# Kernel tuning notes

Measured on AMD Instinct MI355X. Metric: run time of the kernel, lower is better.

Reference implementation:

```python
import jax, jax.numpy as jnp
import numpy as np

W, B, S, D = 4, 1, 1024, 1024   # simulated world_size, batch, local seq, embed_dim
H, DS, HM = 16, 64, 4            # num_heads, summary_dim, meta_heads


def mha(q, k, v, w_in, b_in, w_out, b_out, nheads):
    """torch nn.MultiheadAttention (batch_first). Returns (out, head-averaged weights)."""
    d = q.shape[-1]
    hd = d // nheads
    wq, wk, wv = jnp.split(w_in, 3, axis=0)
    bq, bk, bv = jnp.split(b_in, 3)
    Bq, Sq, _ = q.shape
    Sk = k.shape[1]
    qh = (q @ wq.T + bq).reshape(Bq, Sq, nheads, hd)
    kh = (k @ wk.T + bk).reshape(Bq, Sk, nheads, hd)
    vh = (v @ wv.T + bv).reshape(Bq, Sk, nheads, hd)
    scores = jnp.einsum('bqhd,bkhd->bhqk', qh, kh) / float(np.sqrt(hd))
    attn = jax.nn.softmax(scores, axis=-1)
    out = jnp.einsum('bhqk,bkhd->bqhd', attn, vh).reshape(Bq, Sq, d)
    return out @ w_out.T + b_out, attn.mean(axis=1)


def attn_stats(attn):
    """attn: (B, S) -> (B, 4) [entropy, gini, max, top5]."""
    ent = -(attn * jnp.log(attn + 1e-8)).sum(-1, keepdims=True)
    s = jnp.sort(attn, axis=-1)
    n = attn.shape[-1]
    idx = jnp.arange(1, n + 1, dtype=attn.dtype)
    gini = 2.0 * (idx * s).sum(-1) / (n * s.sum(-1) + 1e-8) - (n + 1) / n
    mx = attn.max(-1, keepdims=True)
    k = min(5, n)
    top5 = jax.lax.top_k(attn, k)[0].sum(-1, keepdims=True)
    return jnp.concatenate([ent, gini[..., None], mx, top5], axis=-1)


def _forward(x, local_in_w, local_in_b, local_out_w, local_out_b,
             sum_query, sum_in_w, sum_in_b, sum_out_w, sum_out_b,
             pat_w1, pat_b1, pat_w2, pat_b2, comb_w, comb_b,
             meta_in_w, meta_in_b, meta_out_w, meta_out_b,
             route_w1, route_b1, route_w2, route_b2,
             cross_in_w, cross_in_b, cross_out_w, cross_out_b,
             gate_w, gate_b, proj_w, proj_b):
    nW = x.shape[0]

    # 1) local attention per rank: (W,B,S,D)
    local = jax.vmap(lambda xc: mha(xc, xc, xc, local_in_w, local_in_b,
                                    local_out_w, local_out_b, H)[0])(x)

    # 2) chunk summary per rank
    def summarize(lo):
        q = jnp.broadcast_to(sum_query, (lo.shape[0], 1, lo.shape[-1]))
        content, w = mha(q, lo, lo, sum_in_w, sum_in_b, sum_out_w, sum_out_b, H)
        content, w = content[:, 0], w[:, 0]              # (B,D), (B,S)
        pat = attn_stats(w)                               # (B,4)
        pat = jax.nn.relu(pat @ pat_w1.T + pat_b1) @ pat_w2.T + pat_b2
        return jnp.concatenate([content, pat], axis=-1) @ comb_w.T + comb_b

    summaries = jax.vmap(summarize)(local)                # (W,B,DS)
    all_sum = jnp.transpose(summaries, (1, 0, 2))         # (B,W,DS) = all-gather

    # 3) meta attention over chunk summaries -> routing weights
    refined, chunk_attn = mha(all_sum, all_sum, all_sum,
                              meta_in_w, meta_in_b, meta_out_w, meta_out_b, HM)
    logits = (jax.nn.relu(refined @ route_w1.T + route_b1) @ route_w2.T + route_b2)[..., 0]
    routing = jax.nn.softmax(logits, axis=-1)             # (B,W)

    all_chunks = jnp.transpose(local, (1, 0, 2, 3))       # (B,W,S,D) = all-gather

    # 4) selective cross-attention + gated combine, per rank
    def per_rank(r, lo):
        rm = routing * (1.0 - jax.nn.one_hot(r, nW, dtype=routing.dtype))
        rm = rm / (rm.sum(-1, keepdims=True) + 1e-8)
        kv = jnp.einsum('bw,bwsd->bsd', rm, all_chunks)
        cross, _ = mha(lo, kv, kv, cross_in_w, cross_in_b, cross_out_w, cross_out_b, H)
        g = jax.nn.sigmoid(jnp.concatenate([lo, cross], axis=-1) @ gate_w.T + gate_b)
        comb = g * cross + (1.0 - g) * lo
        return comb @ proj_w.T + proj_b

    out = jax.vmap(per_rank)(jnp.arange(nW), local)       # (W,B,S,D)
    return out


def setup_inputs() -> dict:
    key = jax.random.key(0)
    ks = iter(jax.random.split(key, 40))
    p = lambda *shape: jax.random.normal(next(ks), shape, dtype=jnp.float32) * 0.02
    inp = {
        'x': jax.random.normal(next(ks), (W, B, S, D), dtype=jnp.float32),
        'local_in_w': p(3 * D, D), 'local_in_b': p(3 * D),
        'local_out_w': p(D, D), 'local_out_b': p(D),
        'sum_query': p(1, 1, D),
        'sum_in_w': p(3 * D, D), 'sum_in_b': p(3 * D),
        'sum_out_w': p(D, D), 'sum_out_b': p(D),
        'pat_w1': p(DS, 4), 'pat_b1': p(DS),
        'pat_w2': p(DS, DS), 'pat_b2': p(DS),
        'comb_w': p(DS, D + DS), 'comb_b': p(DS),
        'meta_in_w': p(3 * DS, DS), 'meta_in_b': p(3 * DS),
        'meta_out_w': p(DS, DS), 'meta_out_b': p(DS),
        'route_w1': p(DS, DS), 'route_b1': p(DS),
        'route_w2': p(1, DS), 'route_b2': p(1),
        'cross_in_w': p(3 * D, D), 'cross_in_b': p(3 * D),
        'cross_out_w': p(D, D), 'cross_out_b': p(D),
        'gate_w': p(D, 2 * D), 'gate_b': p(D),
        'proj_w': p(D, D), 'proj_b': p(D),
    }
    return inp


def reference(x, local_in_w, local_in_b, local_out_w, local_out_b,
              sum_query, sum_in_w, sum_in_b, sum_out_w, sum_out_b,
              pat_w1, pat_b1, pat_w2, pat_b2, comb_w, comb_b,
              meta_in_w, meta_in_b, meta_out_w, meta_out_b,
              route_w1, route_b1, route_w2, route_b2,
              cross_in_w, cross_in_b, cross_out_w, cross_out_b,
              gate_w, gate_b, proj_w, proj_b):
    return _forward(x, local_in_w, local_in_b, local_out_w, local_out_b,
                    sum_query, sum_in_w, sum_in_b, sum_out_w, sum_out_b,
                    pat_w1, pat_b1, pat_w2, pat_b2, comb_w, comb_b,
                    meta_in_w, meta_in_b, meta_out_w, meta_out_b,
                    route_w1, route_b1, route_w2, route_b2,
                    cross_in_w, cross_in_b, cross_out_w, cross_out_b,
                    gate_w, gate_b, proj_w, proj_b)
```

## Files before the change

### kernel.cpp

```cpp
#include <hip/hip_runtime.h>
#include <hip/hip_bf16.h>
#include <stdint.h>

typedef uint16_t u16;
typedef __attribute__((ext_vector_type(8))) short short8;
typedef __attribute__((ext_vector_type(8))) unsigned short ushort8;
typedef __attribute__((ext_vector_type(4))) float f32x4;

#define AS1 __attribute__((address_space(1)))
#define AS3 __attribute__((address_space(3)))

__device__ __forceinline__ float b2f(u16 u){
  union{uint32_t i; float f;} v; v.i=((uint32_t)u)<<16; return v.f;
}
__device__ __forceinline__ u16 f2b(float f){
  union{uint32_t i; float f;} v; v.f=f;
  return (u16)((v.i + 0x7fffu + ((v.i>>16)&1u))>>16);
}
__device__ __forceinline__ u16 f2bf(float f){
  __hip_bfloat16 h = __float2bfloat16(f);
  return *reinterpret_cast<u16*>(&h);
}

struct CvtP { const float* src[8]; u16* dst[8]; long n[8]; };
__global__ void cvt_multi(CvtP p) {
  const int seg = blockIdx.y;
  const long i = ((long)blockIdx.x*256 + threadIdx.x)*8;
  if (i >= p.n[seg]) return;
  const float* in = p.src[seg];
  float4 a = *(const float4*)&in[i];
  float4 b = *(const float4*)&in[i+4];
  ushort8 o;
  o[0]=f2b(a.x); o[1]=f2b(a.y); o[2]=f2b(a.z); o[3]=f2b(a.w);
  o[4]=f2b(b.x); o[5]=f2b(b.y); o[6]=f2b(b.z); o[7]=f2b(b.w);
  *(ushort8*)&p.dst[seg][i] = o;
}

struct GemmP {
  const u16* A; const u16* B; u16* C; const float* bias;
  const u16* B2; u16* C2; const float* bias2;
  long lda, ldb, ldc, ldb2, ldc2;
  int K, Nstore, Nstore2, ySplit, act, outf;
  float scale;
};

__global__ __launch_bounds__(512) void gemm_nt(GemmP p) {
  __shared__ __align__(16) u16 lA[2][4096];
  __shared__ __align__(16) u16 lB[2][4096];
  const int t = threadIdx.x;
  const int wave = t >> 6, lane = t & 63;
  int by = blockIdx.y;
  const u16* Bp; u16* Cp; const float* bias; long ldb, ldc; int nst;
  if (by >= p.ySplit) {
    by -= p.ySplit; Bp = p.B2; Cp = p.C2; bias = p.bias2;
    ldb = p.ldb2; ldc = p.ldc2; nst = p.Nstore2;
  } else {
    Bp = p.B; Cp = p.C; bias = p.bias; ldb = p.ldb; ldc = p.ldc; nst = p.Nstore;
  }
  const u16* A = p.A + (long)blockIdx.x * 128 * p.lda;
  const u16* B = Bp + (long)by * 128 * ldb;
  const int srow = t >> 2, skk = (t & 3) * 8;
  const int wr = wave >> 2, wc = wave & 3;
  const int fr = lane & 15, fk = (lane >> 4) * 8;
  f32x4 acc[4][2] = {};

  __builtin_amdgcn_global_load_lds((const AS1 void*)(A + (long)srow*p.lda + skk),
                                   (AS3 void*)&lA[0][t*8], 16, 0, 0);
  __builtin_amdgcn_global_load_lds((const AS1 void*)(B + (long)srow*ldb + skk),
                                   (AS3 void*)&lB[0][t*8], 16, 0, 0);
  __syncthreads();
  int cur = 0;
  for (int k0 = 0; k0 < p.K; k0 += 32) {
    if (k0 + 32 < p.K) {
      const int nb = cur ^ 1, kn = k0 + 32;
      __builtin_amdgcn_global_load_lds((const AS1 void*)(A + (long)srow*p.lda + kn + skk),
                                       (AS3 void*)&lA[nb][t*8], 16, 0, 0);
      __builtin_amdgcn_global_load_lds((const AS1 void*)(B + (long)srow*ldb + kn + skk),
                                       (AS3 void*)&lB[nb][t*8], 16, 0, 0);
    }
    short8 av[4], bv[2];
    #pragma unroll
    for (int mi = 0; mi < 4; ++mi) av[mi] = *(const short8*)&lA[cur][(wr*64 + mi*16 + fr)*32 + fk];
    #pragma unroll
    for (int ni = 0; ni < 2; ++ni) bv[ni] = *(const short8*)&lB[cur][(wc*32 + ni*16 + fr)*32 + fk];
    #pragma unroll
    for (int mi = 0; mi < 4; ++mi)
      #pragma unroll
      for (int ni = 0; ni < 2; ++ni)
        acc[mi][ni] = __builtin_amdgcn_mfma_f32_16x16x32_bf16(av[mi], bv[ni], acc[mi][ni], 0, 0, 0);
    __syncthreads();
    cur ^= 1;
  }

  const int rbase = blockIdx.x*128 + wr*64;
  const int cbase = by*128 + wc*32;
  const int rsub = (lane >> 4) * 4;
  #pragma unroll
  for (int ni = 0; ni < 2; ++ni) {
    const int col = cbase + ni*16 + fr;
    if (col >= nst) continue;
    const float bs = bias ? bias[col] : 0.f;
    #pragma unroll
    for (int mi = 0; mi < 4; ++mi) {
      #pragma unroll
      for (int j = 0; j < 4; ++j) {
        float v = acc[mi][ni][j] * p.scale + bs;
        if (p.act == 1) v = 1.f / (1.f + __expf(-v));
        const long idx = (long)(rbase + mi*16 + rsub + j) * ldc + col;
        if (p.outf) ((float*)Cp)[idx] = v;
        else        Cp[idx] = f2b(v);
      }
    }
  }
}

struct FlashP {
  const u16 *q, *k, *v; u16* o;
  long ldq, ldkv, ldo;
  long qB, kvB, oB;
};

__global__ __launch_bounds__(256) void flash_k(FlashP p) {
  const int t = threadIdx.x, w4 = t >> 6, lane = t & 63;
  const int qt = blockIdx.x, h = blockIdx.y, wz = blockIdx.z;
  const int fr = lane & 15, g = lane >> 4, fk = g * 8;
  __shared__ __align__(16) u16 kt[64][72];
  __shared__ __align__(16) u16 vt[64][72];
  __shared__ __align__(16) u16 pl[4][16][72];

  const u16* Q = p.q + (long)wz*p.qB + (long)(qt*64 + w4*16)*p.ldq + h*64;
  const u16* K = p.k + (long)wz*p.kvB + h*64;
  const u16* V = p.v + (long)wz*p.kvB + h*64;

  short8 aq[2];
  aq[0] = *(const short8*)&Q[(long)fr*p.ldq + fk];
  aq[1] = *(const short8*)&Q[(long)fr*p.ldq + 32 + fk];

  f32x4 acc[4] = {};
  float mst[4], lst[4];
  #pragma unroll
  for (int j = 0; j < 4; ++j) { mst[j] = -3e38f; lst[j] = 0.f; }

  const int krow = t >> 2, kseg = (t & 3) * 16;
  const int vp = t & 31, vc = (t >> 5) * 8;

  short8 kr0, kr1, vr0, vr1;
  kr0 = *(const short8*)&K[(long)krow*p.ldkv + kseg];
  kr1 = *(const short8*)&K[(long)krow*p.ldkv + kseg + 8];
  vr0 = *(const short8*)&V[(long)(2*vp)*p.ldkv + vc];
  vr1 = *(const short8*)&V[(long)(2*vp + 1)*p.ldkv + vc];

  for (int it = 0; it < 16; ++it) {
    *(short8*)&kt[krow][kseg]     = kr0;
    *(short8*)&kt[krow][kseg + 8] = kr1;
    #pragma unroll
    for (int e = 0; e < 8; ++e) {
      const uint32_t pk = (uint32_t)(uint16_t)vr0[e] | ((uint32_t)(uint16_t)vr1[e] << 16);
      *(uint32_t*)&vt[vc + e][2*vp] = pk;
    }
    __syncthreads();

    if (it + 1 < 16) {
      const int kn = (it + 1) * 64;
      kr0 = *(const short8*)&K[(long)(kn + krow)*p.ldkv + kseg];
      kr1 = *(const short8*)&K[(long)(kn + krow)*p.ldkv + kseg + 8];
      vr0 = *(const short8*)&V[(long)(kn + 2*vp)*p.ldkv + vc];
      vr1 = *(const short8*)&V[(long)(kn + 2*vp + 1)*p.ldkv + vc];
    }

    f32x4 s[4] = {};
    __builtin_amdgcn_s_setprio(1);
    #pragma unroll
    for (int ni = 0; ni < 4; ++ni) {
      short8 bk0 = *(const short8*)&kt[ni*16 + fr][fk];
      short8 bk1 = *(const short8*)&kt[ni*16 + fr][32 + fk];
      s[ni] = __builtin_amdgcn_mfma_f32_16x16x32_bf16(aq[0], bk0, s[ni], 0, 0, 0);
      s[ni] = __builtin_amdgcn_mfma_f32_16x16x32_bf16(aq[1], bk1, s[ni], 0, 0, 0);
    }
    __builtin_amdgcn_s_setprio(0);
    #pragma unroll
    for (int ni = 0; ni < 4; ++ni) s[ni] *= 0.125f;

    #pragma unroll
    for (int j = 0; j < 4; ++j) {
      float rm = fmaxf(fmaxf(s[0][j], s[1][j]), fmaxf(s[2][j], s[3][j]));
      #pragma unroll
      for (int o = 8; o; o >>= 1) rm = fmaxf(rm, __shfl_xor(rm, o, 64));
      const float mnew = fmaxf(mst[j], rm);
      const float alpha = __expf(mst[j] - mnew);
      float rs = 0.f;
      #pragma unroll
      for (int ni = 0; ni < 4; ++ni) {
        const float pv = __expf(s[ni][j] - mnew);
        s[ni][j] = pv;
        rs += pv;
      }
      #pragma unroll
      for (int o = 8; o; o >>= 1) rs += __shfl_xor(rs, o, 64);
      lst[j] = lst[j]*alpha + rs;
      mst[j] = mnew;
      #pragma unroll
      for (int nv = 0; nv < 4; ++nv) acc[nv][j] *= alpha;
    }

    #pragma unroll
    for (int ni = 0; ni < 4; ++ni)
      #pragma unroll
      for (int j = 0; j < 4; ++j)
        pl[w4][g*4 + j][ni*16 + fr] = f2bf(s[ni][j]);

    __builtin_amdgcn_s_setprio(1);
    #pragma unroll
    for (int ks = 0; ks < 2; ++ks) {
      short8 pa = *(const short8*)&pl[w4][fr][ks*32 + fk];
      #pragma unroll
      for (int nv = 0; nv < 4; ++nv) {
        short8 bvv = *(const short8*)&vt[nv*16 + fr][ks*32 + fk];
        acc[nv] = __builtin_amdgcn_mfma_f32_16x16x32_bf16(pa, bvv, acc[nv], 0, 0, 0);
      }
    }
    __builtin_amdgcn_s_setprio(0);
    __syncthreads();
  }

  u16* O = p.o + (long)wz*p.oB + (long)(qt*64 + w4*16)*p.ldo + h*64;
  #pragma unroll
  for (int j = 0; j < 4; ++j) {
    const float inv = 1.f / lst[j];
    #pragma unroll
    for (int nv = 0; nv < 4; ++nv)
      O[(long)(g*4 + j)*p.ldo + nv*16 + fr] = f2bf(acc[nv][j] * inv);
  }
}

__global__ void gemv_qs(const float* sq, const float* w, const float* b, float* out) {
  const int t = threadIdx.x, nl = t & 63, kq = t >> 6;
  const int n = blockIdx.x*64 + nl;
  const float* row = w + (long)n * 1024 + kq*256;
  const float* q = sq + kq*256;
  float s = 0.f;
  for (int k = 0; k < 256; k += 4) {
    float4 ww = *(const float4*)&row[k];
    float4 qq = *(const float4*)&q[k];
    s += qq.x*ww.x + qq.y*ww.y + qq.z*ww.z + qq.w*ww.w;
  }
  __shared__ float ps[4][64];
  ps[kq][nl] = s;
  __syncthreads();
  if (t < 64) out[blockIdx.x*64 + t] = ps[0][t]+ps[1][t]+ps[2][t]+ps[3][t] + b[blockIdx.x*64 + t];
}

__global__ void sum_attend(const float* qs, const u16* sumkv, float* content, float* pall) {
  const int h = blockIdx.x, w = blockIdx.y, t = threadIdx.x;
  const int lane = t & 63, wv = t >> 6;
  __shared__ float qsh[64];
  __shared__ float sc[1024];
  __shared__ float rmax[4], rsum[4];
  __shared__ float po[4][64];
  if (t < 64) qsh[t] = qs[h*64 + t];
  __syncthreads();
  const u16* kbase = sumkv + (long)w*2097152 + h*64;
  float e[4];
  float mx = -1e30f;
  #pragma unroll
  for (int j = 0; j < 4; ++j) {
    const int k = j*256 + t;
    const u16* krow = kbase + (long)k * 2048;
    float s = 0.f;
    #pragma unroll
    for (int d = 0; d < 64; d += 8) {
      ushort8 kk = *(const ushort8*)&krow[d];
      #pragma unroll
      for (int q = 0; q < 8; ++q) s += qsh[d+q] * b2f(kk[q]);
    }
    s *= 0.125f;
    e[j] = s;
    mx = fmaxf(mx, s);
  }
  #pragma unroll
  for (int o = 32; o; o >>= 1) mx = fmaxf(mx, __shfl_xor(mx, o, 64));
  if (lane == 0) rmax[wv] = mx;
  __syncthreads();
  mx = fmaxf(fmaxf(rmax[0],rmax[1]), fmaxf(rmax[2],rmax[3]));
  float sum = 0.f;
  #pragma unroll
  for (int j = 0; j < 4; ++j) { e[j] = __expf(e[j]-mx); sum += e[j]; }
  #pragma unroll
  for (int o = 32; o; o >>= 1) sum += __shfl_xor(sum, o, 64);
  if (lane == 0) rsum[wv] = sum;
  __syncthreads();
  const float inv = 1.f / (rsum[0]+rsum[1]+rsum[2]+rsum[3]);
  float* pr = pall + ((long)w*16 + h)*1024;
  #pragma unroll
  for (int j = 0; j < 4; ++j) {
    const int k = j*256 + t;
    const float pn = e[j]*inv;
    sc[k] = pn;
    pr[k] = pn;
  }
  __syncthreads();
  const u16* vbase = sumkv + (long)w*2097152 + 1024 + h*64;
  float o = 0.f;
  const int k0 = wv*256;
  for (int k = k0; k < k0+256; ++k) o += sc[k] * b2f(vbase[(long)k*2048 + lane]);
  po[wv][lane] = o;
  __syncthreads();
  if (t < 64) content[(long)w*1024 + h*64 + t] = po[0][t]+po[1][t]+po[2][t]+po[3][t];
}

__global__ void wavg_k(const float* pall, float* wavg) {
  const int w = blockIdx.y, k = blockIdx.x*256 + threadIdx.x;
  float s = 0.f;
  #pragma unroll
  for (int h = 0; h < 16; ++h) s += pall[((long)w*16 + h)*1024 + k];
  wavg[w*1024 + k] = s * (1.f/16.f);
}

__global__ void contproj_k(const float* content, const float* w_, const float* b, float* out) {
  const int w = blockIdx.y, t = threadIdx.x;
  const int nl = t & 63, kq = t >> 6;
  const int n = blockIdx.x*64 + nl;
  const float* c = content + w*1024 + kq*256;
  const float* row = w_ + (long)n * 1024 + kq*256;
  float s = 0.f;
  for (int k = 0; k < 256; k += 4) {
    float4 ww = *(const float4*)&row[k];
    s += c[k]*ww.x + c[k+1]*ww.y + c[k+2]*ww.z + c[k+3]*ww.w;
  }
  __shared__ float ps[4][64];
  ps[kq][nl] = s;
  __syncthreads();
  if (t < 64) out[w*1024 + blockIdx.x*64 + t] = ps[0][t]+ps[1][t]+ps[2][t]+ps[3][t] + b[blockIdx.x*64 + t];
}

__global__ void stats1_k(const float* wavg, float* part) {
  const int c = blockIdx.x, w = blockIdx.y, t = threadIdx.x;
  __shared__ float a[1024];
  for (int i = t; i < 1024; i += 256) a[i] = wavg[w*1024 + i];
  __syncthreads();
  const int jl = t & 63, iq = t >> 6;
  const int j = c*64 + jl;
  const float aj = a[j];
  int pr = 0;
  const int i0 = iq*256;
  #pragma unroll 8
  for (int i = i0; i < i0+256; ++i) {
    const float ai = a[i];
    pr += (ai < aj) || (ai == aj && i < j);
  }
  __shared__ int prs[4][64];
  prs[iq][jl] = pr;
  __syncthreads();
  if (t < 64) {
    const int rank = 1 + prs[0][jl] + prs[1][jl] + prs[2][jl] + prs[3][jl];
    float ent = -aj * logf(aj + 1e-8f);
    float gnum = (float)rank * aj;
    float ssum = aj;
    float mx = aj;
    float top5 = (rank >= 1020) ? aj : 0.f;
    #pragma unroll
    for (int o = 32; o; o >>= 1) {
      ent += __shfl_xor(ent, o, 64);
      gnum += __shfl_xor(gnum, o, 64);
      ssum += __shfl_xor(ssum, o, 64);
      mx = fmaxf(mx, __shfl_xor(mx, o, 64));
      top5 += __shfl_xor(top5, o, 64);
    }
    if (t == 0) {
      float* pp = part + ((w*16 + c) * 5);
      pp[0]=ent; pp[1]=gnum; pp[2]=ssum; pp[3]=mx; pp[4]=top5;
    }
  }
}

__global__ void stats2_k(const float* part, float* stats) {
  const int w = blockIdx.x, t = threadIdx.x;
  const int c = t & 15, stat = t >> 4;
  float v = 0.f;
  const bool active = stat < 5;
  if (active) v = part[(w*16 + c)*5 + stat];
  #pragma unroll
  for (int o = 8; o; o >>= 1) {
    const float ov = __shfl_xor(v, o, 64);
    v = (stat == 3) ? fmaxf(v, ov) : (v + ov);
  }
  __shared__ float r5[5];
  if (active && c == 0) r5[stat] = v;
  __syncthreads();
  if (t == 0) {
    stats[w*4+0] = r5[0];
    stats[w*4+1] = 2.f*r5[1]/(1024.f*r5[2] + 1e-8f) - 1025.f/1024.f;
    stats[w*4+2] = r5[3];
    stats[w*4+3] = r5[4];
  }
}

__global__ void patsum_k(const float* stats, const float* contprj,
                         const float* pw1, const float* pb1, const float* pw2, const float* pb2,
                         const float* combw, const float* combb, float* summ) {
  const int w = blockIdx.x, t = threadIdx.x;
  const int nl = t & 63, kq = t >> 6;
  __shared__ float p1[64], pat[64];
  __shared__ float ps[4][64];
  __shared__ float ps2[4][64];
  if (t < 64) {
    float s = 0.f;
    #pragma unroll
    for (int k = 0; k < 4; ++k) s += stats[w*4+k] * pw1[t*4+k];
    p1[t] = fmaxf(s + pb1[t], 0.f);
  }
  __syncthreads();
  {
    float s = 0.f;
    const float* rw = pw2 + (long)nl*64 + kq*16;
    const float* pp = p1 + kq*16;
    #pragma unroll
    for (int k = 0; k < 16; ++k) s += pp[k] * rw[k];
    ps[kq][nl] = s;
  }
  __syncthreads();
  if (t < 64) pat[t] = ps[0][t]+ps[1][t]+ps[2][t]+ps[3][t] + pb2[t];
  __syncthreads();
  const float* c = contprj + w*1024;
  const float* row = combw + (long)nl * 1088;
  float s = 0.f;
  const int k0 = kq*272;
  for (int k = k0; k < k0+272; ++k) {
    const float rv = row[k];
    const float cv = (k < 1024) ? c[k] : pat[k-1024];
    s += cv * rv;
  }
  ps2[kq][nl] = s;
  __syncthreads();
  if (t < 64) summ[w*64 + t] = ps2[0][t]+ps2[1][t]+ps2[2][t]+ps2[3][t] + combb[t];
}

__global__ void meta_k(const float* summ, const float* miw, const float* mib,
                       const float* mow, const float* mob, const float* rw1, const float* rb1,
                       const float* rw2, const float* rb2, float* routing) {
  const int t = threadIdx.x;
  __shared__ float qkv[4][192];
  __shared__ float sc[64];
  __shared__ float o[4][64];
  __shared__ float rf[4][64];
  __shared__ float t1[4][64];
  __shared__ float lg[4];
  for (int idx = t; idx < 768; idx += 64) {
    const int w = idx / 192, rrow = idx % 192;
    const float* rw = miw + (long)rrow * 64;
    float s = 0.f;
    for (int k = 0; k < 64; ++k) s += summ[w*64+k] * rw[k];
    qkv[w][rrow] = s + mib[rrow];
  }
  __syncthreads();
  {
    const int h = t >> 4, i = (t >> 2) & 3, j = t & 3;
    float s = 0.f;
    #pragma unroll
    for (int d = 0; d < 16; ++d) s += qkv[i][h*16+d] * qkv[j][64 + h*16+d];
    sc[t] = s * 0.25f;
  }
  __syncthreads();
  if (t < 16) {
    const float a0=sc[t*4], a1=sc[t*4+1], a2=sc[t*4+2], a3=sc[t*4+3];
    const float m = fmaxf(fmaxf(a0,a1), fmaxf(a2,a3));
    const float e0=__expf(a0-m), e1=__expf(a1-m), e2=__expf(a2-m), e3=__expf(a3-m);
    const float s = e0+e1+e2+e3;
    sc[t*4]=e0/s; sc[t*4+1]=e1/s; sc[t*4+2]=e2/s; sc[t*4+3]=e3/s;
  }
  __syncthreads();
  for (int idx = t; idx < 256; idx += 64) {
    const int i = idx >> 6, c = idx & 63, h = c >> 4;
    float s = 0.f;
    #pragma unroll
    for (int j = 0; j < 4; ++j) s += sc[(h*4+i)*4+j] * qkv[j][128 + c];
    o[i][c] = s;
  }
  __syncthreads();
  for (int idx = t; idx < 256; idx += 64) {
    const int i = idx >> 6, n = idx & 63;
    const float* rw = mow + (long)n * 64;
    float s = 0.f;
    for (int k = 0; k < 64; ++k) s += o[i][k] * rw[k];
    rf[i][n] = s + mob[n];
  }
  __syncthreads();
  for (int idx = t; idx < 256; idx += 64) {
    const int i = idx >> 6, n = idx & 63;
    const float* rw = rw1 + (long)n * 64;
    float s = 0.f;
    for (int k = 0; k < 64; ++k) s += rf[i][k] * rw[k];
    t1[i][n] = fmaxf(s + rb1[n], 0.f);
  }
  __syncthreads();
  if (t < 4) {
    float s = 0.f;
    for (int k = 0; k < 64; ++k) s += t1[t][k] * rw2[k];
    lg[t] = s + rb2[0];
  }
  __syncthreads();
  if (t == 0) {
    const float m = fmaxf(fmaxf(lg[0],lg[1]), fmaxf(lg[2],lg[3]));
    float e[4], s = 0.f;
    #pragma unroll
    for (int i = 0; i < 4; ++i) { e[i] = __expf(lg[i]-m); s += e[i]; }
    #pragma unroll
    for (int i = 0; i < 4; ++i) routing[i] = e[i]/s;
  }
}

__global__ void kvr_k(const u16* local, const float* routing, u16* kvr) {
  const int r = blockIdx.y;
  const long e = ((long)blockIdx.x*256 + threadIdx.x) * 8;
  float rm[4]; float s = 0.f;
  #pragma unroll
  for (int w = 0; w < 4; ++w) { rm[w] = (w == r) ? 0.f : routing[w]; s += rm[w]; }
  const float inv = 1.f / (s + 1e-8f);
  ushort8 a0 = *(const ushort8*)&local[e];
  ushort8 a1 = *(const ushort8*)&local[1048576 + e];
  ushort8 a2 = *(const ushort8*)&local[2097152 + e];
  ushort8 a3 = *(const ushort8*)&local[3145728 + e];
  ushort8 out;
  #pragma unroll
  for (int j = 0; j < 8; ++j)
    out[j] = f2b((rm[0]*b2f(a0[j]) + rm[1]*b2f(a1[j]) + rm[2]*b2f(a2[j]) + rm[3]*b2f(a3[j])) * inv);
  *(ushort8*)&kvr[(long)r*1048576 + e] = out;
}

__global__ void gcat_k(const u16* local, const u16* cross, u16* gcat) {
  const long e = ((long)blockIdx.x*256 + threadIdx.x) * 8;
  const long row = e >> 11, col = e & 2047;
  const u16* src = (col < 1024) ? &local[row*1024 + col] : &cross[row*1024 + col - 1024];
  *(ushort8*)&gcat[e] = *(const ushort8*)src;
}

__global__ void comb_k(const u16* g, const u16* cross, const u16* local, u16* comb) {
  const long e = ((long)blockIdx.x*256 + threadIdx.x) * 8;
  ushort8 gg = *(const ushort8*)&g[e];
  ushort8 cc = *(const ushort8*)&cross[e];
  ushort8 ll = *(const ushort8*)&local[e];
  ushort8 out;
  #pragma unroll
  for (int j = 0; j < 8; ++j) {
    const float gf = b2f(gg[j]);
    out[j] = f2b(gf*b2f(cc[j]) + (1.f-gf)*b2f(ll[j]));
  }
  *(ushort8*)&comb[e] = out;
}

static void gemm1(hipStream_t st, dim3 grid,
                  const u16* A, long lda, const u16* B, long ldb,
                  u16* C, long ldc, const float* bias,
                  int K, int N, float scale, int act, int outf) {
  GemmP p = {};
  p.A=A; p.B=B; p.C=C; p.bias=bias;
  p.lda=lda; p.ldb=ldb; p.ldc=ldc;
  p.K=K; p.Nstore=N; p.ySplit=1<<30; p.act=act; p.outf=outf; p.scale=scale;
  gemm_nt<<<grid, dim3(512), 0, st>>>(p);
}

extern "C" void kernel_launch(void* const* d_in, const int* in_sizes, int n_in,
                              void* d_out, int out_size, void* d_ws, size_t ws_size,
                              hipStream_t stream) {
  (void)in_sizes; (void)n_in; (void)out_size; (void)ws_size;
  const float* x   = (const float*)d_in[0];
  const float* liw = (const float*)d_in[1];
  const float* lib = (const float*)d_in[2];
  const float* low = (const float*)d_in[3];
  const float* lob = (const float*)d_in[4];
  const float* sq  = (const float*)d_in[5];
  const float* siw = (const float*)d_in[6];
  const float* sib = (const float*)d_in[7];
  const float* sow = (const float*)d_in[8];
  const float* sob = (const float*)d_in[9];
  const float* pw1 = (const float*)d_in[10];
  const float* pb1 = (const float*)d_in[11];
  const float* pw2 = (const float*)d_in[12];
  const float* pb2 = (const float*)d_in[13];
  const float* cbw = (const float*)d_in[14];
  const float* cbb = (const float*)d_in[15];
  const float* miw = (const float*)d_in[16];
  const float* mib = (const float*)d_in[17];
  const float* mow = (const float*)d_in[18];
  const float* mob = (const float*)d_in[19];
  const float* rw1 = (const float*)d_in[20];
  const float* rb1 = (const float*)d_in[21];
  const float* rw2 = (const float*)d_in[22];
  const float* rb2 = (const float*)d_in[23];
  const float* ciw = (const float*)d_in[24];
  const float* cib = (const float*)d_in[25];
  const float* cow = (const float*)d_in[26];
  const float* cob = (const float*)d_in[27];
  const float* gw  = (const float*)d_in[28];
  const float* gb  = (const float*)d_in[29];
  const float* pw  = (const float*)d_in[30];
  const float* pb  = (const float*)d_in[31];

  char* ws = (char*)d_ws;
  u16* qkv    = (u16*)(ws + 0);
  u16* aout   = (u16*)(ws + 25165824);
  u16* local  = (u16*)(ws + 33554432);
  u16* scratch= (u16*)(ws + 41943040);
  u16* s2048  = (u16*)(ws + 79691776);
  u16* cq     = (u16*)(ws + 96468992);
  u16* kvr    = (u16*)(ws + 104857600);
  u16* crossb = (u16*)(ws + 113246208);
  char* sf = ws + 121634816;
  float* qs      = (float*)(sf + 0);
  float* pall    = (float*)(sf + 4096);
  float* wavg    = (float*)(sf + 266240);
  float* content = (float*)(sf + 282624);
  float* contprj = (float*)(sf + 299008);
  float* stats   = (float*)(sf + 315392);
  float* summ    = (float*)(sf + 315456);
  float* routing = (float*)(sf + 316480);
  float* part    = (float*)(sf + 316544);
  u16* siwkvb = (u16*)(ws + 122028032);
  u16* lowb   = (u16*)(ws + 126222336);
  u16* ciwb   = (u16*)(ws + 128319488);
  u16* cowb   = (u16*)(ws + 134610944);
  u16* gwb    = (u16*)(ws + 136708096);
  u16* pwb    = (u16*)(ws + 140902400);
  u16* xb   = crossb;
  u16* liwb = scratch;

  CvtP cp;
  cp.src[0]=x;   cp.dst[0]=xb;     cp.n[0]=4194304;
  cp.src[1]=liw; cp.dst[1]=liwb;   cp.n[1]=3145728;
  cp.src[2]=low; cp.dst[2]=lowb;   cp.n[2]=1048576;
  cp.src[3]=siw+1048576; cp.dst[3]=siwkvb; cp.n[3]=2097152;
  cp.src[4]=ciw; cp.dst[4]=ciwb;   cp.n[4]=3145728;
  cp.src[5]=cow; cp.dst[5]=cowb;   cp.n[5]=1048576;
  cp.src[6]=gw;  cp.dst[6]=gwb;    cp.n[6]=2097152;
  cp.src[7]=pw;  cp.dst[7]=pwb;    cp.n[7]=1048576;
  cvt_multi<<<dim3(2048, 8), dim3(256), 0, stream>>>(cp);

  gemm1(stream, dim3(32,24), xb,1024, liwb,1024, qkv,3072, lib, 1024, 3072, 1.f, 0, 0);

  {
    FlashP fp;
    fp.q = qkv; fp.k = qkv + 1024; fp.v = qkv + 2048; fp.o = aout;
    fp.ldq = 3072; fp.ldkv = 3072; fp.ldo = 1024;
    fp.qB = 3145728; fp.kvB = 3145728; fp.oB = 1048576;
    flash_k<<<dim3(16,16,4), dim3(256), 0, stream>>>(fp);
  }

  gemm1(stream, dim3(32,8), aout,1024, lowb,1024, local,1024, lob, 1024, 1024, 1.f, 0, 0);

  {
    GemmP p = {};
    p.A = local; p.lda = 1024; p.K = 1024; p.scale = 1.f;
    p.B = ciwb;   p.C = cq;    p.bias = cib;      p.ldb = 1024; p.ldc = 1024; p.Nstore = 1024;
    p.B2 = siwkvb; p.C2 = s2048; p.bias2 = sib+1024; p.ldb2 = 1024; p.ldc2 = 2048; p.Nstore2 = 2048;
    p.ySplit = 8;
    gemm_nt<<<dim3(32,24), dim3(512), 0, stream>>>(p);
  }

  gemv_qs<<<dim3(16), dim3(256), 0, stream>>>(sq, siw, sib, qs);
  sum_attend<<<dim3(16,4), dim3(256), 0, stream>>>(qs, s2048, content, pall);
  wavg_k<<<dim3(4,4), dim3(256), 0, stream>>>(pall, wavg);
  contproj_k<<<dim3(16,4), dim3(256), 0, stream>>>(content, sow, sob, contprj);
  stats1_k<<<dim3(16,4), dim3(256), 0, stream>>>(wavg, part);
  stats2_k<<<dim3(4), dim3(128), 0, stream>>>(part, stats);
  patsum_k<<<dim3(4), dim3(256), 0, stream>>>(stats, contprj, pw1, pb1, pw2, pb2, cbw, cbb, summ);

  meta_k<<<dim3(1), dim3(64), 0, stream>>>(summ, miw, mib, mow, mob, rw1, rb1, rw2, rb2, routing);

  kvr_k<<<dim3(512,4), dim3(256), 0, stream>>>(local, routing, kvr);

  gemm1(stream, dim3(32,16), kvr,1024, ciwb+1048576,1024, s2048,2048, cib+1024, 1024, 2048, 1.f, 0, 0);

  {
    FlashP fp;
    fp.q = cq; fp.k = s2048; fp.v = s2048 + 1024; fp.o = aout;
    fp.ldq = 1024; fp.ldkv = 2048; fp.ldo = 1024;
    fp.qB = 1048576; fp.kvB = 2097152; fp.oB = 1048576;
    flash_k<<<dim3(16,16,4), dim3(256), 0, stream>>>(fp);
  }

  gemm1(stream, dim3(32,8), aout,1024, cowb,1024, crossb,1024, cob, 1024, 1024, 1.f, 0, 0);

  gcat_k<<<dim3(4096), dim3(256), 0, stream>>>(local, crossb, s2048);
  gemm1(stream, dim3(32,8), s2048,2048, gwb,2048, cq,1024, gb, 2048, 1024, 1.f, 1, 0);

  comb_k<<<dim3(2048), dim3(256), 0, stream>>>(cq, crossb, local, kvr);

  gemm1(stream, dim3(32,8), kvr,1024, pwb,1024, (u16*)d_out,1024, pb, 1024, 1024, 1.f, 0, 1);
}
```

Baseline: 463.1 us.

## Transpose QK^T MFMA layout, use exp2 softmax with lazy max rescaling

The QK^T MFMA operands are swapped so each lane holds one query row's scores. The row max and sum then need only two cross-lane shuffles, and P can be stored to shared memory as packed 4-element vectors. Softmax uses exp2 with the scale folded into a single constant. Rescaling of the accumulator is skipped unless some row's max grows by more than a threshold. This removes per-row shuffle reductions, the scaling pass and most alpha multiplies, at the cost of slightly looser overflow headroom in the exponent.

```diff
diff --git a/kernel.cpp b/kernel.cpp
--- a/kernel.cpp
+++ b/kernel.cpp
@@ -4,6 +4,7 @@
 
 typedef uint16_t u16;
 typedef __attribute__((ext_vector_type(8))) short short8;
+typedef __attribute__((ext_vector_type(4))) short short4v;
 typedef __attribute__((ext_vector_type(8))) unsigned short ushort8;
 typedef __attribute__((ext_vector_type(4))) float f32x4;
 
@@ -137,9 +138,8 @@
   aq[1] = *(const short8*)&Q[(long)fr*p.ldq + 32 + fk];
 
   f32x4 acc[4] = {};
-  float mst[4], lst[4];
-  #pragma unroll
-  for (int j = 0; j < 4; ++j) { mst[j] = -3e38f; lst[j] = 0.f; }
+  float ml = -3e38f, ll = 0.f;
+  const float C = 0.125f * 1.44269504f;
 
   const int krow = t >> 2, kseg = (t & 3) * 16;
   const int vp = t & 31, vc = (t >> 5) * 8;
@@ -174,40 +174,56 @@
     for (int ni = 0; ni < 4; ++ni) {
       short8 bk0 = *(const short8*)&kt[ni*16 + fr][fk];
       short8 bk1 = *(const short8*)&kt[ni*16 + fr][32 + fk];
-      s[ni] = __builtin_amdgcn_mfma_f32_16x16x32_bf16(aq[0], bk0, s[ni], 0, 0, 0);
-      s[ni] = __builtin_amdgcn_mfma_f32_16x16x32_bf16(aq[1], bk1, s[ni], 0, 0, 0);
+      s[ni] = __builtin_amdgcn_mfma_f32_16x16x32_bf16(bk0, aq[0], s[ni], 0, 0, 0);
+      s[ni] = __builtin_amdgcn_mfma_f32_16x16x32_bf16(bk1, aq[1], s[ni], 0, 0, 0);
     }
     __builtin_amdgcn_s_setprio(0);
-    #pragma unroll
-    for (int ni = 0; ni < 4; ++ni) s[ni] *= 0.125f;
-
-    #pragma unroll
-    for (int j = 0; j < 4; ++j) {
-      float rm = fmaxf(fmaxf(s[0][j], s[1][j]), fmaxf(s[2][j], s[3][j]));
-      #pragma unroll
-      for (int o = 8; o; o >>= 1) rm = fmaxf(rm, __shfl_xor(rm, o, 64));
-      const float mnew = fmaxf(mst[j], rm);
-      const float alpha = __expf(mst[j] - mnew);
-      float rs = 0.f;
-      #pragma unroll
-      for (int ni = 0; ni < 4; ++ni) {
-        const float pv = __expf(s[ni][j] - mnew);
-        s[ni][j] = pv;
-        rs += pv;
-      }
-      #pragma unroll
-      for (int o = 8; o; o >>= 1) rs += __shfl_xor(rs, o, 64);
-      lst[j] = lst[j]*alpha + rs;
-      mst[j] = mnew;
-      #pragma unroll
-      for (int nv = 0; nv < 4; ++nv) acc[nv][j] *= alpha;
-    }
-
+
+    float rm = s[0][0];
     #pragma unroll
     for (int ni = 0; ni < 4; ++ni)
       #pragma unroll
-      for (int j = 0; j < 4; ++j)
-        pl[w4][g*4 + j][ni*16 + fr] = f2bf(s[ni][j]);
+      for (int j = 0; j < 4; ++j) rm = fmaxf(rm, s[ni][j]);
+    rm = fmaxf(rm, __shfl_xor(rm, 16, 64));
+    rm = fmaxf(rm, __shfl_xor(rm, 32, 64));
+    const float rml = rm * C;
+
+    if (__any(rml > ml + 11.5f)) {
+      const float mnl = fmaxf(ml, rml);
+      const float al = exp2f(ml - mnl);
+      const float a0 = __shfl(al, g*4 + 0, 64);
+      const float a1 = __shfl(al, g*4 + 1, 64);
+      const float a2 = __shfl(al, g*4 + 2, 64);
+      const float a3 = __shfl(al, g*4 + 3, 64);
+      #pragma unroll
+      for (int nv = 0; nv < 4; ++nv) {
+        acc[nv][0] *= a0; acc[nv][1] *= a1; acc[nv][2] *= a2; acc[nv][3] *= a3;
+      }
+      ll *= al;
+      ml = mnl;
+    }
+
+    float rs = 0.f;
+    u16 pb[4][4];
+    #pragma unroll
+    for (int ni = 0; ni < 4; ++ni)
+      #pragma unroll
+      for (int j = 0; j < 4; ++j) {
+        const float pv = exp2f(s[ni][j]*C - ml);
+        rs += pv;
+        pb[ni][j] = f2bf(pv);
+      }
+    rs += __shfl_xor(rs, 16, 64);
+    rs += __shfl_xor(rs, 32, 64);
+    ll += rs;
+
+    #pragma unroll
+    for (int ni = 0; ni < 4; ++ni) {
+      short4v pk4;
+      pk4[0] = (short)pb[ni][0]; pk4[1] = (short)pb[ni][1];
+      pk4[2] = (short)pb[ni][2]; pk4[3] = (short)pb[ni][3];
+      *(short4v*)&pl[w4][fr][ni*16 + g*4] = pk4;
+    }
 
     __builtin_amdgcn_s_setprio(1);
     #pragma unroll
@@ -223,14 +239,17 @@
     __syncthreads();
   }
 
+  const float l0 = __shfl(ll, g*4 + 0, 64);
+  const float l1 = __shfl(ll, g*4 + 1, 64);
+  const float l2 = __shfl(ll, g*4 + 2, 64);
+  const float l3 = __shfl(ll, g*4 + 3, 64);
+  const float inv[4] = {1.f/l0, 1.f/l1, 1.f/l2, 1.f/l3};
   u16* O = p.o + (long)wz*p.oB + (long)(qt*64 + w4*16)*p.ldo + h*64;
   #pragma unroll
-  for (int j = 0; j < 4; ++j) {
-    const float inv = 1.f / lst[j];
+  for (int j = 0; j < 4; ++j)
     #pragma unroll
     for (int nv = 0; nv < 4; ++nv)
-      O[(long)(g*4 + j)*p.ldo + nv*16 + fr] = f2bf(acc[nv][j] * inv);
-  }
+      O[(long)(g*4 + j)*p.ldo + nv*16 + fr] = f2bf(acc[nv][j] * inv[j]);
 }
 
 __global__ void gemv_qs(const float* sq, const float* w, const float* b, float* out) {
```

After: 433.2 us. 6.5% less time.
